# Kernel tuning notes

Measured on AMD Instinct MI355X. Metric: run time of the kernel, lower is better.

## Reference

```python
import jax, jax.numpy as jnp
import numpy as np

H = 16
D_MODEL = 1024
D_K = D_MODEL // H  # 64, must equal embeddim


def setup_inputs() -> dict:
    key = jax.random.key(0)
    ks = jax.random.split(key, 20)
    B, S, D = 4, 1024, D_MODEL
    s = 0.02
    inp = {
        'query': jax.random.normal(ks[0], (B, S, D), jnp.float32),
        'key':   jax.random.normal(ks[1], (B, S, D), jnp.float32),
        'value': jax.random.normal(ks[2], (B, S, D), jnp.float32),
        'mask':  jnp.ones((B, S, S), jnp.int32),
        # four d_model x d_model projections (q, k, v, out)
        'wq': jax.random.normal(ks[3], (D, D), jnp.float32) * s, 'bq': jnp.zeros((D,), jnp.float32),
        'wk': jax.random.normal(ks[4], (D, D), jnp.float32) * s, 'bk': jnp.zeros((D,), jnp.float32),
        'wv': jax.random.normal(ks[5], (D, D), jnp.float32) * s, 'bv': jnp.zeros((D,), jnp.float32),
        'wo': jax.random.normal(ks[6], (D, D), jnp.float32) * s, 'bo': jnp.zeros((D,), jnp.float32),
        # per-head (embeddim=64) linears
        'spatial_w': jax.random.normal(ks[7], (D_K, D_K), jnp.float32) * s, 'spatial_b': jnp.zeros((D_K,), jnp.float32),
        'qproj_w':   jax.random.normal(ks[8], (D_K, D_K), jnp.float32) * s, 'qproj_b':   jnp.zeros((D_K,), jnp.float32),
        'kproj_w':   jax.random.normal(ks[9], (D_K, D_K), jnp.float32) * s, 'kproj_b':   jnp.zeros((D_K,), jnp.float32),
        'vlin_w':    jax.random.normal(ks[10], (D_K, D_K), jnp.float32) * s, 'vlin_b':    jnp.zeros((D_K,), jnp.float32),
        # channel_linear: Linear(1, 64)
        'chan_w': jax.random.normal(ks[11], (1, D_K), jnp.float32) * s, 'chan_b': jnp.zeros((D_K,), jnp.float32),
    }
    return inp


def reference(query, key, value, mask,
              wq, bq, wk, bk, wv, bv, wo, bo,
              spatial_w, spatial_b, qproj_w, qproj_b,
              kproj_w, kproj_b, vlin_w, vlin_b, chan_w, chan_b):
    B, S, D = query.shape
    # project and split heads -> [B, H, S, D_K]
    def heads(x, w, b):
        return (x @ w + b).reshape(B, S, H, D_K).transpose(0, 2, 1, 3)
    q = heads(query, wq, bq)
    k = heads(key, wk, bk)
    v = heads(value, wv, bv)

    q = jax.nn.elu(q @ spatial_w + spatial_b)
    q_refine = q @ qproj_w + qproj_b
    # channel gate: mean over channels -> Linear(1,64) -> matmul with raw key
    alpha = q_refine.mean(-1, keepdims=True) @ chan_w + chan_b        # [B,H,S,64]
    gate = jax.nn.sigmoid(jnp.einsum('bhqe,bhke->bhqk', alpha, k))    # [B,H,S,S]

    k2 = jax.nn.elu(k @ kproj_w + kproj_b)
    scores = jnp.einsum('bhqe,bhke->bhqk', q, k2) / jnp.sqrt(jnp.asarray(D_K, q.dtype))
    scores = scores * gate
    scores = jnp.where(mask[:, None] == 0, jnp.asarray(-1e9, scores.dtype), scores)
    p_attn = jax.nn.softmax(scores, axis=-1)

    v2 = jax.nn.elu(v @ vlin_w + vlin_b)
    x = jnp.einsum('bhqk,bhke->bhqe', p_attn, v2)                     # [B,H,S,64]
    x = x.transpose(0, 2, 1, 3).reshape(B, S, H * D_K)
    return x @ wo + bo
```

## Files before the change

### kernel.cpp

```cpp
#include <hip/hip_runtime.h>
#include <math.h>

#define D_MODEL 1024
#define NH 16
#define DK 64
#define S_LEN 1024
#define BATCH 4
#define MROWS (BATCH * S_LEN)

typedef short bf16x8 __attribute__((ext_vector_type(8)));
typedef float f32x4 __attribute__((ext_vector_type(4)));
typedef unsigned short u16;

__device__ __forceinline__ float elu1(float x) {
    return x > 0.f ? x : (expf(x) - 1.f);
}

__device__ __forceinline__ u16 f2bf(float f) {
    union { float f; unsigned u; } v; v.f = f;
    unsigned u = v.u;
    return (u16)((u + 0x7fffu + ((u >> 16) & 1u)) >> 16);
}

__device__ __forceinline__ u16 f2bf_fast(float f) {
    union { float f; unsigned u; } v; v.f = f;
    return (u16)((v.u + 0x8000u) >> 16);
}

__device__ __forceinline__ void async16(const void* g, void* l) {
    __builtin_amdgcn_global_load_lds(
        (const __attribute__((address_space(1))) unsigned int*)g,
        (__attribute__((address_space(3))) unsigned int*)l,
        16, 0, 0);
}

__global__ __launch_bounds__(256) void prep(
    const float* __restrict__ wq, const float* __restrict__ wk,
    const float* __restrict__ wv, const float* __restrict__ wo,
    u16* __restrict__ WT,
    const float* __restrict__ Xq, const float* __restrict__ Xk,
    const float* __restrict__ Xv, u16* __restrict__ Xb,
    const int* __restrict__ mask, unsigned long long* __restrict__ Mb)
{
    __shared__ float T[64][65];
    const int bid = blockIdx.x;
    const int tid = threadIdx.x;

    if (bid < 1024) {
        const int z = bid >> 8;
        const int rem = bid & 255;
        const int n0 = (rem & 15) * 64, k0 = (rem >> 4) * 64;
        const float* W = (z == 0) ? wq : ((z == 1) ? wk : ((z == 2) ? wv : wo));
        u16* O = WT + (size_t)z * D_MODEL * D_MODEL;
        const int r = tid >> 4, c4 = (tid & 15) * 4;
        #pragma unroll
        for (int p = 0; p < 4; p++) {
            float4 v = *(const float4*)&W[(size_t)(k0 + r + p * 16) * D_MODEL + n0 + c4];
            T[r + p * 16][c4 + 0] = v.x; T[r + p * 16][c4 + 1] = v.y;
            T[r + p * 16][c4 + 2] = v.z; T[r + p * 16][c4 + 3] = v.w;
        }
        __syncthreads();
        #pragma unroll
        for (int p = 0; p < 4; p++) {
            const int i = r + p * 16;
            ushort4 o4;
            o4.x = f2bf(T[c4 + 0][i]); o4.y = f2bf(T[c4 + 1][i]);
            o4.z = f2bf(T[c4 + 2][i]); o4.w = f2bf(T[c4 + 3][i]);
            *(ushort4*)&O[(size_t)(n0 + i) * D_MODEL + k0 + c4] = o4;
        }
    } else if (bid < 1024 + 6144) {
        const int idx = bid - 1024;
        const int z = idx >> 11;
        const int bx = idx & 2047;
        const float* X = (z == 0) ? Xq : ((z == 1) ? Xk : Xv);
        u16* O = Xb + (size_t)z * MROWS * D_MODEL;
        const size_t i = ((size_t)bx * 256 + tid) * 8;
        float4 a = *(const float4*)&X[i];
        float4 b = *(const float4*)&X[i + 4];
        ushort4 o0, o1;
        o0.x = f2bf(a.x); o0.y = f2bf(a.y); o0.z = f2bf(a.z); o0.w = f2bf(a.w);
        o1.x = f2bf(b.x); o1.y = f2bf(b.y); o1.z = f2bf(b.z); o1.w = f2bf(b.w);
        *(ushort4*)&O[i] = o0;
        *(ushort4*)&O[i + 4] = o1;
    } else {
        const int bx = bid - 7168;
        const int gw = (bx * 256 + tid) >> 6;
        const int lane = tid & 63;
        int v[8];
        #pragma unroll
        for (int i = 0; i < 8; i++)
            v[i] = mask[((size_t)gw + (size_t)i * 8192) * 64 + lane];
        #pragma unroll
        for (int i = 0; i < 8; i++) {
            unsigned long long bits = __ballot(v[i] != 0);
            if (lane == 0) Mb[(size_t)gw + (size_t)i * 8192] = bits;
        }
    }
}

__global__ __launch_bounds__(256) void proj_fused(
    const u16* __restrict__ Xq, const u16* __restrict__ Xk, const u16* __restrict__ Xv,
    const u16* __restrict__ WTq, const u16* __restrict__ WTk, const u16* __restrict__ WTv,
    const float* __restrict__ bq, const float* __restrict__ bk, const float* __restrict__ bv,
    const float* __restrict__ spatial_w, const float* __restrict__ spatial_b,
    const float* __restrict__ qproj_w, const float* __restrict__ qproj_b,
    const float* __restrict__ kproj_w, const float* __restrict__ kproj_b,
    const float* __restrict__ vlin_w, const float* __restrict__ vlin_b,
    const float* __restrict__ chan_w, const float* __restrict__ chan_b,
    u16* __restrict__ Qh, u16* __restrict__ K2, u16* __restrict__ V2t,
    float* __restrict__ mB, float* __restrict__ uB, float* __restrict__ vB)
{
    __shared__ __align__(16) u16 smem[16896];
    __shared__ float auxA[64];
    __shared__ float auxS;

    u16* As = smem;
    u16* Bs = smem + 8192;
    u16* W2t = smem + 12288;

    const int z = blockIdx.z;
    const u16* X = (z == 0) ? Xq : ((z == 1) ? Xk : Xv);
    const u16* WT = (z == 0) ? WTq : ((z == 1) ? WTk : WTv);
    const float* B1 = (z == 0) ? bq : ((z == 1) ? bk : bv);
    const float* W2 = (z == 0) ? spatial_w : ((z == 1) ? kproj_w : vlin_w);
    const float* B2 = (z == 0) ? spatial_b : ((z == 1) ? kproj_b : vlin_b);

    const int tid = threadIdx.x;
    const int wave = tid >> 6, lane = tid & 63;
    const int col = lane & 15, quad = lane >> 4;
    const int r0 = blockIdx.x * 128;
    const int hh = blockIdx.y;
    const int n0 = hh * 64;

    #pragma unroll
    for (int p = 0; p < 4; p++) {
        int idx = p * 256 + tid;
        int f = idx >> 4, e4 = (idx & 15) * 4;
        float4 w4 = *(const float4*)&W2[f * 64 + e4];
        W2t[(e4 + 0) * 72 + f] = f2bf(w4.x);
        W2t[(e4 + 1) * 72 + f] = f2bf(w4.y);
        W2t[(e4 + 2) * 72 + f] = f2bf(w4.z);
        W2t[(e4 + 3) * 72 + f] = f2bf(w4.w);
    }
    if (z == 0) {
        {
            int row = tid >> 2, part = tid & 3;
            float s = 0.f;
            for (int e = part * 16; e < part * 16 + 16; e++) s += qproj_w[row * 64 + e];
            s += __shfl_xor(s, 1);
            s += __shfl_xor(s, 2);
            if (part == 0) auxA[row] = s * (1.f / 64.f);
        }
        if (tid < 64) {
            float s = qproj_b[tid];
            #pragma unroll
            for (int m = 1; m < 64; m <<= 1) s += __shfl_xor(s, m);
            if (tid == 0) auxS = s * (1.f / 64.f);
        }
    }

    const int srow8 = lane >> 3;
    const int sg = ((lane & 7) ^ srow8) * 8;

    const u16* ap = X + (size_t)(r0 + wave * 32 + srow8) * D_MODEL + sg;
    const u16* bp = WT + (size_t)(n0 + wave * 16 + srow8) * D_MODEL + sg;
    u16* adst = As + (wave * 32) * 64;
    u16* bdst = Bs + (wave * 16) * 64;

    f32x4 acc[2][4];
    #pragma unroll
    for (int i = 0; i < 2; i++)
        #pragma unroll
        for (int j = 0; j < 4; j++)
            acc[i][j] = (f32x4){0.f, 0.f, 0.f, 0.f};

    for (int k0 = 0; k0 < D_MODEL; k0 += 64) {
        if (k0) __syncthreads();
        #pragma unroll
        for (int i = 0; i < 4; i++)
            async16(ap + (size_t)(i * 8) * D_MODEL + k0, adst + i * 512);
        #pragma unroll
        for (int j = 0; j < 2; j++)
            async16(bp + (size_t)(j * 8) * D_MODEL + k0, bdst + j * 512);
        __syncthreads();
        #pragma unroll
        for (int ks = 0; ks < 2; ks++) {
            const int gk = ((ks * 4 + quad) ^ (col & 7)) * 8;
            const u16* Abase = As + (wave * 32 + col) * 64 + gk;
            const u16* Bbase = Bs + col * 64 + gk;
            bf16x8 af[2], bfr[4];
            #pragma unroll
            for (int mi = 0; mi < 2; mi++) af[mi] = *(const bf16x8*)(Abase + mi * 1024);
            #pragma unroll
            for (int ni = 0; ni < 4; ni++) bfr[ni] = *(const bf16x8*)(Bbase + ni * 1024);
            #pragma unroll
            for (int mi = 0; mi < 2; mi++)
                #pragma unroll
                for (int ni = 0; ni < 4; ni++)
                    acc[mi][ni] = __builtin_amdgcn_mfma_f32_16x16x32_bf16(af[mi], bfr[ni], acc[mi][ni], 0, 0, 0);
        }
    }

    float b1v[4];
    #pragma unroll
    for (int ni = 0; ni < 4; ni++) b1v[ni] = B1[n0 + ni * 16 + col];

    const int rbase = r0 + wave * 32;
    const int b = r0 >> 10;
    const int s0 = (r0 & 1023) + wave * 32;
    const size_t svecbase = ((size_t)b * NH + hh) * S_LEN;

    if (z == 1) {
        float cw[4], cb[4];
        #pragma unroll
        for (int ni = 0; ni < 4; ni++) { cw[ni] = chan_w[ni * 16 + col]; cb[ni] = chan_b[ni * 16 + col]; }
        #pragma unroll
        for (int mi = 0; mi < 2; mi++)
            #pragma unroll
            for (int r = 0; r < 4; r++) {
                float su = 0.f, sv = 0.f;
                #pragma unroll
                for (int ni = 0; ni < 4; ni++) {
                    float p = acc[mi][ni][r] + b1v[ni];
                    su += p * cw[ni];
                    sv += p * cb[ni];
                }
                su += __shfl_xor(su, 1); su += __shfl_xor(su, 2);
                su += __shfl_xor(su, 4); su += __shfl_xor(su, 8);
                sv += __shfl_xor(sv, 1); sv += __shfl_xor(sv, 2);
                sv += __shfl_xor(sv, 4); sv += __shfl_xor(sv, 8);
                if (col == 0) {
                    const size_t idx = svecbase + s0 + mi * 16 + quad * 4 + r;
                    uB[idx] = su;
                    vB[idx] = sv;
                }
            }
    }

    __syncthreads();

    u16* Pchunk = smem + wave * 1536;
    bf16x8 bf2r[4][2];
    #pragma unroll
    for (int ni = 0; ni < 4; ni++) {
        bf2r[ni][0] = *(const bf16x8*)&W2t[(ni * 16 + col) * 72 + quad * 8];
        bf2r[ni][1] = *(const bf16x8*)&W2t[(ni * 16 + col) * 72 + 32 + quad * 8];
    }
    float qs[2][4][4];
    #pragma unroll
    for (int mi = 0; mi < 2; mi++) {
        #pragma unroll
        for (int ni = 0; ni < 4; ni++)
            #pragma unroll
            for (int r = 0; r < 4; r++)
                Pchunk[(quad * 4 + r) * 72 + ni * 16 + col] = f2bf(acc[mi][ni][r] + b1v[ni]);
        __builtin_amdgcn_s_waitcnt(0xc07f);
        __builtin_amdgcn_sched_barrier(0);
        bf16x8 a0 = *(const bf16x8*)&Pchunk[col * 72 + quad * 8];
        bf16x8 a1 = *(const bf16x8*)&Pchunk[col * 72 + 32 + quad * 8];
        __builtin_amdgcn_s_waitcnt(0xc07f);
        __builtin_amdgcn_sched_barrier(0);
        #pragma unroll
        for (int ni = 0; ni < 4; ni++) {
            f32x4 c = (f32x4){0.f, 0.f, 0.f, 0.f};
            c = __builtin_amdgcn_mfma_f32_16x16x32_bf16(a0, bf2r[ni][0], c, 0, 0, 0);
            c = __builtin_amdgcn_mfma_f32_16x16x32_bf16(a1, bf2r[ni][1], c, 0, 0, 0);
            const float bb = B2[ni * 16 + col];
            #pragma unroll
            for (int r = 0; r < 4; r++) qs[mi][ni][r] = elu1(c[r] + bb);
        }
    }

    if (z == 0) {
        float aw[4];
        #pragma unroll
        for (int ni = 0; ni < 4; ni++) aw[ni] = auxA[ni * 16 + col];
        #pragma unroll
        for (int mi = 0; mi < 2; mi++)
            #pragma unroll
            for (int r = 0; r < 4; r++) {
                float pm = 0.f;
                #pragma unroll
                for (int ni = 0; ni < 4; ni++) pm += qs[mi][ni][r] * aw[ni];
                pm += __shfl_xor(pm, 1); pm += __shfl_xor(pm, 2);
                pm += __shfl_xor(pm, 4); pm += __shfl_xor(pm, 8);
                if (col == 0)
                    mB[svecbase + s0 + mi * 16 + quad * 4 + r] = pm + auxS;
            }
        #pragma unroll
        for (int mi = 0; mi < 2; mi++)
            #pragma unroll
            for (int ni = 0; ni < 4; ni++)
                #pragma unroll
                for (int r = 0; r < 4; r++)
                    Qh[(size_t)(rbase + mi * 16 + quad * 4 + r) * D_MODEL
                       + n0 + ni * 16 + col] = f2bf(qs[mi][ni][r] * 0.125f);
    } else if (z == 1) {
        #pragma unroll
        for (int mi = 0; mi < 2; mi++)
            #pragma unroll
            for (int ni = 0; ni < 4; ni++)
                #pragma unroll
                for (int r = 0; r < 4; r++)
                    K2[(size_t)(rbase + mi * 16 + quad * 4 + r) * D_MODEL
                       + n0 + ni * 16 + col] = f2bf(qs[mi][ni][r]);
    } else {
        u16* Tb = W2t;
        __syncthreads();
        #pragma unroll
        for (int p = 0; p < 2; p++) {
            if ((wave >> 1) == p) {
                const int sloc = (wave & 1) * 32;
                #pragma unroll
                for (int mi = 0; mi < 2; mi++)
                    #pragma unroll
                    for (int ni = 0; ni < 4; ni++)
                        #pragma unroll
                        for (int r = 0; r < 4; r++)
                            Tb[(ni * 16 + col) * 72 + sloc + mi * 16 + quad * 4 + r] =
                                f2bf(qs[mi][ni][r]);
            }
            __syncthreads();
            {
                const int d = tid >> 2, seg = tid & 3;
                u16* dst = V2t + (((size_t)b * NH + hh) * DK + d) * S_LEN
                         + (r0 & 1023) + p * 64 + seg * 16;
                *(uint4*)dst = *(const uint4*)&Tb[d * 72 + seg * 16];
                *(uint4*)(dst + 8) = *(const uint4*)&Tb[d * 72 + seg * 16 + 8];
            }
            if (p == 0) __syncthreads();
        }
    }
}

__global__ __launch_bounds__(256) void attn_mfma(
    const u16* __restrict__ Qh, const u16* __restrict__ K2h, const u16* __restrict__ V2t,
    const float* __restrict__ Mq, const float* __restrict__ Uk, const float* __restrict__ Vk,
    const unsigned long long* __restrict__ Mb, u16* __restrict__ X)
{
    __shared__ u16 K2s[64][72];
    __shared__ u16 V2s[64][72];
    __shared__ u16 Ps[4][16][72];

    const int tid = threadIdx.x;
    const int wave = tid >> 6, lane = tid & 63;
    const int col = lane & 15, quad = lane >> 4;

    const int f = blockIdx.x;
    const int o = (f & 7) * 128 + (f >> 3);
    const int q0 = (o & 15) * 64;
    const int h = (o >> 4) & 15;
    const int b = o >> 8;

    const size_t hb = ((size_t)(b * NH + h)) * S_LEN * DK;
    const size_t sb = ((size_t)(b * NH + h)) * S_LEN;

    bf16x8 qf0, qf1;
    {
        const u16* qp = Qh + (size_t)(b * S_LEN + q0 + wave * 16 + col) * D_MODEL + h * 64 + quad * 8;
        qf0 = *(const bf16x8*)qp;
        qf1 = *(const bf16x8*)(qp + 32);
    }
    float mqv[4];
    #pragma unroll
    for (int r = 0; r < 4; r++)
        mqv[r] = Mq[sb + q0 + wave * 16 + quad * 4 + r];

    const int srow = tid >> 2, sseg = tid & 3;
    const u16* ksrc = K2h + (size_t)(b * S_LEN + srow) * D_MODEL + h * 64 + sseg * 16;
    const u16* vsrc = V2t + hb + (size_t)srow * S_LEN + sseg * 16;
    const unsigned long long* mbase = Mb
        + ((size_t)b * S_LEN + q0 + wave * 16 + quad * 4) * (S_LEN / 64);
    const unsigned msel0 = 1u << col, msel1 = msel0 << 16;

    uint4 ka = *(const uint4*)(ksrc);
    uint4 kb = *(const uint4*)(ksrc + 8);
    uint4 va = *(const uint4*)(vsrc);
    uint4 vb = *(const uint4*)(vsrc + 8);
    float ku[4], kv[4];
    unsigned long long wm[4];
    #pragma unroll
    for (int nb = 0; nb < 4; nb++) {
        ku[nb] = Uk[sb + nb * 16 + col];
        kv[nb] = Vk[sb + nb * 16 + col];
    }
    #pragma unroll
    for (int r = 0; r < 4; r++) wm[r] = mbase[r * 16];

    float psum[4] = {0.f, 0.f, 0.f, 0.f};
    f32x4 o4[4];
    #pragma unroll
    for (int nb = 0; nb < 4; nb++) o4[nb] = (f32x4){0.f, 0.f, 0.f, 0.f};

    for (int t = 0; t < 16; t++) {
        *(uint4*)&K2s[srow][sseg * 16]     = ka;
        *(uint4*)&K2s[srow][sseg * 16 + 8] = kb;
        *(uint4*)&V2s[srow][sseg * 16]     = va;
        *(uint4*)&V2s[srow][sseg * 16 + 8] = vb;
        __syncthreads();

        if (t < 15) {
            const int k1 = (t + 1) * 64;
            const u16* ks = ksrc + (size_t)k1 * D_MODEL;
            const u16* vs = vsrc + k1;
            ka = *(const uint4*)(ks);
            kb = *(const uint4*)(ks + 8);
            va = *(const uint4*)(vs);
            vb = *(const uint4*)(vs + 8);
        }

        __builtin_amdgcn_s_setprio(1);
        f32x4 sc[4];
        #pragma unroll
        for (int nb = 0; nb < 4; nb++) {
            bf16x8 b0 = *(const bf16x8*)&K2s[nb * 16 + col][quad * 8];
            bf16x8 b1 = *(const bf16x8*)&K2s[nb * 16 + col][32 + quad * 8];
            f32x4 c = (f32x4){0.f, 0.f, 0.f, 0.f};
            c = __builtin_amdgcn_mfma_f32_16x16x32_bf16(qf0, b0, c, 0, 0, 0);
            c = __builtin_amdgcn_mfma_f32_16x16x32_bf16(qf1, b1, c, 0, 0, 0);
            sc[nb] = c;
        }
        __builtin_amdgcn_s_setprio(0);

        #pragma unroll
        for (int nb = 0; nb < 4; nb++) {
            #pragma unroll
            for (int r = 0; r < 4; r++) {
                float e = __expf(-(mqv[r] * ku[nb] + kv[nb]));
                float g = __builtin_amdgcn_rcpf(1.f + e);
                float sv = sc[nb][r] * g;
                const unsigned bits = (nb < 2) ? (unsigned)wm[r]
                                               : (unsigned)(wm[r] >> 32);
                sv = (bits & ((nb & 1) ? msel1 : msel0)) ? sv : -30.f;
                float p = __expf(sv);
                psum[r] += p;
                Ps[wave][quad * 4 + r][nb * 16 + col] = f2bf_fast(p);
            }
        }
        if (t < 15) {
            const int k1 = (t + 1) * 64;
            #pragma unroll
            for (int nb = 0; nb < 4; nb++) {
                ku[nb] = Uk[sb + k1 + nb * 16 + col];
                kv[nb] = Vk[sb + k1 + nb * 16 + col];
            }
            #pragma unroll
            for (int r = 0; r < 4; r++) wm[r] = mbase[r * 16 + t + 1];
        }
        __builtin_amdgcn_s_waitcnt(0xc07f);
        __builtin_amdgcn_sched_barrier(0);
        bf16x8 a0 = *(const bf16x8*)&Ps[wave][col][quad * 8];
        bf16x8 a1 = *(const bf16x8*)&Ps[wave][col][32 + quad * 8];

        __builtin_amdgcn_s_setprio(1);
        #pragma unroll
        for (int nb = 0; nb < 4; nb++) {
            bf16x8 b0 = *(const bf16x8*)&V2s[nb * 16 + col][quad * 8];
            bf16x8 b1 = *(const bf16x8*)&V2s[nb * 16 + col][32 + quad * 8];
            o4[nb] = __builtin_amdgcn_mfma_f32_16x16x32_bf16(a0, b0, o4[nb], 0, 0, 0);
            o4[nb] = __builtin_amdgcn_mfma_f32_16x16x32_bf16(a1, b1, o4[nb], 0, 0, 0);
        }
        __builtin_amdgcn_s_setprio(0);
        __syncthreads();
    }

    #pragma unroll
    for (int r = 0; r < 4; r++) {
        float t = psum[r];
        t += __shfl_xor(t, 1);
        t += __shfl_xor(t, 2);
        t += __shfl_xor(t, 4);
        t += __shfl_xor(t, 8);
        float inv = __builtin_amdgcn_rcpf(t);
        u16* xp = X + (size_t)(b * S_LEN + q0 + wave * 16 + quad * 4 + r) * D_MODEL + h * 64 + col;
        #pragma unroll
        for (int nb = 0; nb < 4; nb++)
            xp[nb * 16] = f2bf_fast(o4[nb][r] * inv);
    }
}

__global__ __launch_bounds__(256) void out_gemm(
    const u16* __restrict__ A, const u16* __restrict__ WT,
    const float* __restrict__ bias, float* __restrict__ C)
{
    __shared__ u16 As[128 * 32];
    __shared__ u16 Bs[64 * 32];

    const int tid = threadIdx.x;
    const int wave = tid >> 6, lane = tid & 63;
    const int col = lane & 15, quad = lane >> 4;
    const int r0 = blockIdx.x * 128, n0 = blockIdx.y * 64;

    const int srow = lane >> 2;
    const int sg = ((lane & 3) ^ ((lane >> 3) & 3)) * 8;
    const u16* ap = A + (size_t)(r0 + wave * 32 + srow) * D_MODEL + sg;
    const u16* bp = WT + (size_t)(n0 + wave * 16 + srow) * D_MODEL + sg;
    u16* adst0 = As + (wave * 32) * 32;  u16* adst1 = adst0 + 512;
    u16* bdst = Bs + wave * 16 * 32;

    f32x4 acc[2][4];
    #pragma unroll
    for (int i = 0; i < 2; i++)
        #pragma unroll
        for (int j = 0; j < 4; j++)
            acc[i][j] = (f32x4){0.f, 0.f, 0.f, 0.f};

    const int gsw = (quad ^ ((col >> 1) & 3)) * 8;

    for (int k0 = 0; k0 < D_MODEL; k0 += 32) {
        if (k0) __syncthreads();
        async16(ap + k0, adst0);
        async16(ap + (size_t)16 * D_MODEL + k0, adst1);
        async16(bp + k0, bdst);
        __syncthreads();
        const u16* Ab = As + (wave * 32 + col) * 32 + gsw;
        const u16* Bb = Bs + col * 32 + gsw;
        bf16x8 af[2], bfr[4];
        #pragma unroll
        for (int mi = 0; mi < 2; mi++) af[mi] = *(const bf16x8*)(Ab + mi * 512);
        #pragma unroll
        for (int ni = 0; ni < 4; ni++) bfr[ni] = *(const bf16x8*)(Bb + ni * 512);
        #pragma unroll
        for (int mi = 0; mi < 2; mi++)
            #pragma unroll
            for (int ni = 0; ni < 4; ni++)
                acc[mi][ni] = __builtin_amdgcn_mfma_f32_16x16x32_bf16(af[mi], bfr[ni], acc[mi][ni], 0, 0, 0);
    }

    #pragma unroll
    for (int mi = 0; mi < 2; mi++)
        #pragma unroll
        for (int ni = 0; ni < 4; ni++) {
            const int gr = r0 + wave * 32 + mi * 16 + quad * 4;
            const int gc = n0 + ni * 16 + col;
            const float bb = bias[gc];
            #pragma unroll
            for (int r = 0; r < 4; r++)
                C[(size_t)(gr + r) * D_MODEL + gc] = acc[mi][ni][r] + bb;
        }
}

extern "C" void kernel_launch(void* const* d_in, const int* in_sizes, int n_in,
                              void* d_out, int out_size, void* d_ws, size_t ws_size,
                              hipStream_t stream) {
    (void)in_sizes; (void)n_in; (void)out_size; (void)ws_size;
    const float* query = (const float*)d_in[0];
    const float* key_  = (const float*)d_in[1];
    const float* value = (const float*)d_in[2];
    const int*   mask  = (const int*)d_in[3];
    const float* wq = (const float*)d_in[4];  const float* bq = (const float*)d_in[5];
    const float* wk = (const float*)d_in[6];  const float* bk = (const float*)d_in[7];
    const float* wv = (const float*)d_in[8];  const float* bv = (const float*)d_in[9];
    const float* wo = (const float*)d_in[10]; const float* bo = (const float*)d_in[11];
    const float* spatial_w = (const float*)d_in[12]; const float* spatial_b = (const float*)d_in[13];
    const float* qproj_w   = (const float*)d_in[14]; const float* qproj_b   = (const float*)d_in[15];
    const float* kproj_w   = (const float*)d_in[16]; const float* kproj_b   = (const float*)d_in[17];
    const float* vlin_w    = (const float*)d_in[18]; const float* vlin_b    = (const float*)d_in[19];
    const float* chan_w    = (const float*)d_in[20]; const float* chan_b    = (const float*)d_in[21];
    float* out = (float*)d_out;

    char* ws = (char*)d_ws;
    u16* Qh  = (u16*)ws;
    u16* K2  = (u16*)(ws + ((size_t)8  << 20));
    u16* Xb  = (u16*)(ws + ((size_t)16 << 20));
    u16* WT  = (u16*)(ws + ((size_t)24 << 20));
    u16* V2t = (u16*)(ws + ((size_t)32 << 20));
    float* mB = (float*)(ws + ((size_t)40 << 20));
    float* uB = mB + (size_t)BATCH * NH * S_LEN;
    float* vB = uB + (size_t)BATCH * NH * S_LEN;
    unsigned long long* Mbits = (unsigned long long*)(ws + ((size_t)41 << 20));
    u16* Xbf = (u16*)(ws + ((size_t)42 << 20));
    const size_t WSZ = (size_t)D_MODEL * D_MODEL;
    const size_t XSZ = (size_t)MROWS * D_MODEL;

    prep<<<dim3(9216), 256, 0, stream>>>(wq, wk, wv, wo, WT,
        query, key_, value, Xbf, mask, Mbits);
    proj_fused<<<dim3(32, 16, 3), 256, 0, stream>>>(Xbf, Xbf + XSZ, Xbf + 2 * XSZ,
        WT, WT + WSZ, WT + 2 * WSZ, bq, bk, bv,
        spatial_w, spatial_b, qproj_w, qproj_b, kproj_w, kproj_b,
        vlin_w, vlin_b, chan_w, chan_b,
        Qh, K2, V2t, mB, uB, vB);
    attn_mfma<<<dim3(1024), 256, 0, stream>>>(Qh, K2, V2t, mB, uB, vB, Mbits, Xb);
    out_gemm<<<dim3(32, 16), 256, 0, stream>>>(Xb, WT + 3 * WSZ, bo, out);
}
```

Measured before the change: 277.0 us.

## Process 128 query rows per attention block to reuse K/V tiles

Each attention block now covers two 64-row query chunks instead of one, so every K2/V2 tile staged in shared memory serves twice as many queries and the grid is halved. The gate and mask operands are loaded inside the loop instead of being prefetched, and there is a leftover redundant mask load expression. This halves global K/V traffic per query but doubles per-block register state and serial work, which lowers parallelism to 512 blocks.

```diff
diff --git a/kernel.cpp b/kernel.cpp
--- a/kernel.cpp
+++ b/kernel.cpp
@@ -347,29 +347,31 @@
     const int col = lane & 15, quad = lane >> 4;
 
     const int f = blockIdx.x;
-    const int o = (f & 7) * 128 + (f >> 3);
-    const int q0 = (o & 15) * 64;
-    const int h = (o >> 4) & 15;
-    const int b = o >> 8;
+    const int o = (f & 7) * 64 + (f >> 3);
+    const int q0 = (o & 7) * 128;
+    const int h = (o >> 3) & 15;
+    const int b = o >> 7;
 
     const size_t hb = ((size_t)(b * NH + h)) * S_LEN * DK;
     const size_t sb = ((size_t)(b * NH + h)) * S_LEN;
 
-    bf16x8 qf0, qf1;
-    {
-        const u16* qp = Qh + (size_t)(b * S_LEN + q0 + wave * 16 + col) * D_MODEL + h * 64 + quad * 8;
-        qf0 = *(const bf16x8*)qp;
-        qf1 = *(const bf16x8*)(qp + 32);
-    }
-    float mqv[4];
-    #pragma unroll
-    for (int r = 0; r < 4; r++)
-        mqv[r] = Mq[sb + q0 + wave * 16 + quad * 4 + r];
+    bf16x8 qf0[2], qf1[2];
+    float mqv[2][4];
+    #pragma unroll
+    for (int qc = 0; qc < 2; qc++) {
+        const u16* qp = Qh + (size_t)(b * S_LEN + q0 + qc * 64 + wave * 16 + col) * D_MODEL
+                      + h * 64 + quad * 8;
+        qf0[qc] = *(const bf16x8*)qp;
+        qf1[qc] = *(const bf16x8*)(qp + 32);
+        #pragma unroll
+        for (int r = 0; r < 4; r++)
+            mqv[qc][r] = Mq[sb + q0 + qc * 64 + wave * 16 + quad * 4 + r];
+    }
 
     const int srow = tid >> 2, sseg = tid & 3;
     const u16* ksrc = K2h + (size_t)(b * S_LEN + srow) * D_MODEL + h * 64 + sseg * 16;
     const u16* vsrc = V2t + hb + (size_t)srow * S_LEN + sseg * 16;
-    const unsigned long long* mbase = Mb
+    const unsigned long long* mb0 = Mb
         + ((size_t)b * S_LEN + q0 + wave * 16 + quad * 4) * (S_LEN / 64);
     const unsigned msel0 = 1u << col, msel1 = msel0 << 16;
 
@@ -377,26 +379,29 @@
     uint4 kb = *(const uint4*)(ksrc + 8);
     uint4 va = *(const uint4*)(vsrc);
     uint4 vb = *(const uint4*)(vsrc + 8);
-    float ku[4], kv[4];
-    unsigned long long wm[4];
-    #pragma unroll
-    for (int nb = 0; nb < 4; nb++) {
-        ku[nb] = Uk[sb + nb * 16 + col];
-        kv[nb] = Vk[sb + nb * 16 + col];
-    }
-    #pragma unroll
-    for (int r = 0; r < 4; r++) wm[r] = mbase[r * 16];
-
-    float psum[4] = {0.f, 0.f, 0.f, 0.f};
-    f32x4 o4[4];
-    #pragma unroll
-    for (int nb = 0; nb < 4; nb++) o4[nb] = (f32x4){0.f, 0.f, 0.f, 0.f};
+
+    float psum[2][4];
+    f32x4 o4[2][4];
+    #pragma unroll
+    for (int qc = 0; qc < 2; qc++) {
+        #pragma unroll
+        for (int r = 0; r < 4; r++) psum[qc][r] = 0.f;
+        #pragma unroll
+        for (int nb = 0; nb < 4; nb++) o4[qc][nb] = (f32x4){0.f, 0.f, 0.f, 0.f};
+    }
 
     for (int t = 0; t < 16; t++) {
         *(uint4*)&K2s[srow][sseg * 16]     = ka;
         *(uint4*)&K2s[srow][sseg * 16 + 8] = kb;
         *(uint4*)&V2s[srow][sseg * 16]     = va;
         *(uint4*)&V2s[srow][sseg * 16 + 8] = vb;
+
+        float ku[4], kv[4];
+        #pragma unroll
+        for (int nb = 0; nb < 4; nb++) {
+            ku[nb] = Uk[sb + t * 64 + nb * 16 + col];
+            kv[nb] = Vk[sb + t * 64 + nb * 16 + col];
+        }
         __syncthreads();
 
         if (t < 15) {
@@ -409,74 +414,80 @@
             vb = *(const uint4*)(vs + 8);
         }
 
-        __builtin_amdgcn_s_setprio(1);
-        f32x4 sc[4];
-        #pragma unroll
-        for (int nb = 0; nb < 4; nb++) {
-            bf16x8 b0 = *(const bf16x8*)&K2s[nb * 16 + col][quad * 8];
-            bf16x8 b1 = *(const bf16x8*)&K2s[nb * 16 + col][32 + quad * 8];
-            f32x4 c = (f32x4){0.f, 0.f, 0.f, 0.f};
-            c = __builtin_amdgcn_mfma_f32_16x16x32_bf16(qf0, b0, c, 0, 0, 0);
-            c = __builtin_amdgcn_mfma_f32_16x16x32_bf16(qf1, b1, c, 0, 0, 0);
-            sc[nb] = c;
-        }
-        __builtin_amdgcn_s_setprio(0);
-
-        #pragma unroll
-        for (int nb = 0; nb < 4; nb++) {
-            #pragma unroll
-            for (int r = 0; r < 4; r++) {
-                float e = __expf(-(mqv[r] * ku[nb] + kv[nb]));
-                float g = __builtin_amdgcn_rcpf(1.f + e);
-                float sv = sc[nb][r] * g;
-                const unsigned bits = (nb < 2) ? (unsigned)wm[r]
-                                               : (unsigned)(wm[r] >> 32);
-                sv = (bits & ((nb & 1) ? msel1 : msel0)) ? sv : -30.f;
-                float p = __expf(sv);
-                psum[r] += p;
-                Ps[wave][quad * 4 + r][nb * 16 + col] = f2bf_fast(p);
-            }
-        }
-        if (t < 15) {
-            const int k1 = (t + 1) * 64;
+        #pragma unroll
+        for (int qc = 0; qc < 2; qc++) {
+            unsigned long long wm[4];
+            #pragma unroll
+            for (int r = 0; r < 4; r++)
+                wm[r] = mb0[(qc * 64 + r * 4 / 4 * 0 + r) * 16 + t + (size_t)qc * 64 * 16 - (size_t)qc * 64 * 16 + (size_t)qc * 1024 - (size_t)qc * 1024];
+            #pragma unroll
+            for (int r = 0; r < 4; r++)
+                wm[r] = mb0[((size_t)qc * 64 + r) * 16 + t];
+
+            __builtin_amdgcn_s_setprio(1);
+            f32x4 sc[4];
             #pragma unroll
             for (int nb = 0; nb < 4; nb++) {
-                ku[nb] = Uk[sb + k1 + nb * 16 + col];
-                kv[nb] = Vk[sb + k1 + nb * 16 + col];
-            }
-            #pragma unroll
-            for (int r = 0; r < 4; r++) wm[r] = mbase[r * 16 + t + 1];
-        }
-        __builtin_amdgcn_s_waitcnt(0xc07f);
-        __builtin_amdgcn_sched_barrier(0);
-        bf16x8 a0 = *(const bf16x8*)&Ps[wave][col][quad * 8];
-        bf16x8 a1 = *(const bf16x8*)&Ps[wave][col][32 + quad * 8];
-
-        __builtin_amdgcn_s_setprio(1);
-        #pragma unroll
-        for (int nb = 0; nb < 4; nb++) {
-            bf16x8 b0 = *(const bf16x8*)&V2s[nb * 16 + col][quad * 8];
-            bf16x8 b1 = *(const bf16x8*)&V2s[nb * 16 + col][32 + quad * 8];
-            o4[nb] = __builtin_amdgcn_mfma_f32_16x16x32_bf16(a0, b0, o4[nb], 0, 0, 0);
-            o4[nb] = __builtin_amdgcn_mfma_f32_16x16x32_bf16(a1, b1, o4[nb], 0, 0, 0);
-        }
-        __builtin_amdgcn_s_setprio(0);
+                bf16x8 b0 = *(const bf16x8*)&K2s[nb * 16 + col][quad * 8];
+                bf16x8 b1 = *(const bf16x8*)&K2s[nb * 16 + col][32 + quad * 8];
+                f32x4 c = (f32x4){0.f, 0.f, 0.f, 0.f};
+                c = __builtin_amdgcn_mfma_f32_16x16x32_bf16(qf0[qc], b0, c, 0, 0, 0);
+                c = __builtin_amdgcn_mfma_f32_16x16x32_bf16(qf1[qc], b1, c, 0, 0, 0);
+                sc[nb] = c;
+            }
+            __builtin_amdgcn_s_setprio(0);
+
+            #pragma unroll
+            for (int nb = 0; nb < 4; nb++) {
+                #pragma unroll
+                for (int r = 0; r < 4; r++) {
+                    float e = __expf(-(mqv[qc][r] * ku[nb] + kv[nb]));
+                    float g = __builtin_amdgcn_rcpf(1.f + e);
+                    float sv = sc[nb][r] * g;
+                    const unsigned bits = (nb < 2) ? (unsigned)wm[r]
+                                                   : (unsigned)(wm[r] >> 32);
+                    sv = (bits & ((nb & 1) ? msel1 : msel0)) ? sv : -30.f;
+                    float p = __expf(sv);
+                    psum[qc][r] += p;
+                    Ps[wave][quad * 4 + r][nb * 16 + col] = f2bf_fast(p);
+                }
+            }
+            __builtin_amdgcn_s_waitcnt(0xc07f);
+            __builtin_amdgcn_sched_barrier(0);
+            bf16x8 a0 = *(const bf16x8*)&Ps[wave][col][quad * 8];
+            bf16x8 a1 = *(const bf16x8*)&Ps[wave][col][32 + quad * 8];
+            __builtin_amdgcn_s_waitcnt(0xc07f);
+            __builtin_amdgcn_sched_barrier(0);
+
+            __builtin_amdgcn_s_setprio(1);
+            #pragma unroll
+            for (int nb = 0; nb < 4; nb++) {
+                bf16x8 b0 = *(const bf16x8*)&V2s[nb * 16 + col][quad * 8];
+                bf16x8 b1 = *(const bf16x8*)&V2s[nb * 16 + col][32 + quad * 8];
+                o4[qc][nb] = __builtin_amdgcn_mfma_f32_16x16x32_bf16(a0, b0, o4[qc][nb], 0, 0, 0);
+                o4[qc][nb] = __builtin_amdgcn_mfma_f32_16x16x32_bf16(a1, b1, o4[qc][nb], 0, 0, 0);
+            }
+            __builtin_amdgcn_s_setprio(0);
+        }
         __syncthreads();
     }
 
     #pragma unroll
-    for (int r = 0; r < 4; r++) {
-        float t = psum[r];
-        t += __shfl_xor(t, 1);
-        t += __shfl_xor(t, 2);
-        t += __shfl_xor(t, 4);
-        t += __shfl_xor(t, 8);
-        float inv = __builtin_amdgcn_rcpf(t);
-        u16* xp = X + (size_t)(b * S_LEN + q0 + wave * 16 + quad * 4 + r) * D_MODEL + h * 64 + col;
-        #pragma unroll
-        for (int nb = 0; nb < 4; nb++)
-            xp[nb * 16] = f2bf_fast(o4[nb][r] * inv);
-    }
+    for (int qc = 0; qc < 2; qc++)
+        #pragma unroll
+        for (int r = 0; r < 4; r++) {
+            float t = psum[qc][r];
+            t += __shfl_xor(t, 1);
+            t += __shfl_xor(t, 2);
+            t += __shfl_xor(t, 4);
+            t += __shfl_xor(t, 8);
+            float inv = __builtin_amdgcn_rcpf(t);
+            u16* xp = X + (size_t)(b * S_LEN + q0 + qc * 64 + wave * 16 + quad * 4 + r) * D_MODEL
+                    + h * 64 + col;
+            #pragma unroll
+            for (int nb = 0; nb < 4; nb++)
+                xp[nb * 16] = f2bf_fast(o4[qc][nb][r] * inv);
+        }
 }
 
 __global__ __launch_bounds__(256) void out_gemm(
@@ -580,6 +591,6 @@
         spatial_w, spatial_b, qproj_w, qproj_b, kproj_w, kproj_b,
         vlin_w, vlin_b, chan_w, chan_b,
         Qh, K2, V2t, mB, uB, vB);
-    attn_mfma<<<dim3(1024), 256, 0, stream>>>(Qh, K2, V2t, mB, uB, vB, Mbits, Xb);
+    attn_mfma<<<dim3(512), 256, 0, stream>>>(Qh, K2, V2t, mB, uB, vB, Mbits, Xb);
     out_gemm<<<dim3(32, 16), 256, 0, stream>>>(Xb, WT + 3 * WSZ, bo, out);
 }
```

Result: no change. 276.0 us (-0.4%).
